# Performance work log

Measured on AMD Instinct MI355X. Metric: run time of the kernel, lower is better.

Reference implementation:

```python
import jax, jax.numpy as jnp
import numpy as np

B, S, H, E, V, OOV = 64, 400, 512, 256, 50000, 100

def setup_inputs() -> dict:
    key = jax.random.key(0)
    ks = jax.random.split(key, 32)
    p = lambda i, shape: jax.random.normal(ks[i], shape, jnp.float32) * 0.02
    emb = p(0, (V, E)).at[0].set(0.0)  # padding_idx=0
    return dict(
        summaries_in=jax.random.randint(ks[1], (B,), 1, V),
        h0=jax.random.normal(ks[2], (B, H), jnp.float32),
        c0=jax.random.normal(ks[3], (B, H), jnp.float32),
        encoder_out=jax.random.normal(ks[4], (B, S, 2 * H), jnp.float32),
        encoder_features=jax.random.normal(ks[5], (S * B, 2 * H), jnp.float32),
        encoder_mask=jnp.ones((S, B), jnp.float32),
        context=jax.random.normal(ks[6], (B, 2 * H), jnp.float32),
        coverage=jax.random.uniform(ks[7], (S, B), jnp.float32) * 0.01,
        texts_extended=jax.random.randint(ks[8], (S, B), 0, V + OOV),
        oov_size=OOV,
        emb=emb,
        W_feat=p(10, (2 * H, 2 * H)), b_feat=p(11, (2 * H,)),
        W_cov=p(12, (2 * H,)), b_cov=p(13, (2 * H,)),
        w_att=p(14, (2 * H,)), b_att=p(15, ()),
        W_ih=p(16, (4 * H, E)), W_hh=p(17, (4 * H, H)),
        b_ih=p(18, (4 * H,)), b_hh=p(19, (4 * H,)),
        W_ctx=p(20, (E, 2 * H + E)), b_ctx=p(21, (E,)),
        W_pg=p(22, (4 * H + E,)), b_pg=p(23, ()),
        W_o1=p(24, (H, 3 * H)), b_o1=p(25, (H,)),
        W_o2=p(26, (V, H)), b_o2=p(27, (V,)),
    )


def reference(summaries_in, h0, c0, encoder_out, encoder_features, encoder_mask,
              context, coverage, texts_extended, oov_size, emb,
              W_feat, b_feat, W_cov, b_cov, w_att, b_att,
              W_ih, W_hh, b_ih, b_hh, W_ctx, b_ctx, W_pg, b_pg,
              W_o1, b_o1, W_o2, b_o2):
    # embedding + context projection: [B, 2H+E] -> [B, E]
    x = emb[summaries_in]
    ctx_out = jnp.concatenate([context, x], axis=1) @ W_ctx.T + b_ctx
    # single LSTM step (torch gate order i, f, g, o)
    gates = ctx_out @ W_ih.T + b_ih + h0 @ W_hh.T + b_hh
    i, f, g, o = jnp.split(gates, 4, axis=1)
    c = jax.nn.sigmoid(f) * c0 + jax.nn.sigmoid(i) * jnp.tanh(g)
    h = jax.nn.sigmoid(o) * jnp.tanh(c)
    hidden_out = jnp.concatenate([h, c], axis=1)  # [B, 2H]
    # Bahdanau attention with coverage
    dec_feat = hidden_out @ W_feat.T + b_feat                 # [B, 2H]
    ef = encoder_features.reshape(S, B, 2 * H)                # [S, B, 2H]
    cov_feat = coverage[..., None] * W_cov + b_cov            # Linear(1, 2H)
    e = jnp.tanh(ef + dec_feat[None] + cov_feat) @ w_att + b_att  # [S, B]
    a = jax.nn.softmax(e, axis=0) * encoder_mask
    a = a / jnp.sum(a, axis=0, keepdims=True)                 # renormalize (Normalize(0))
    ctx_new = jnp.einsum('sb,bsd->bd', a, encoder_out)        # [B, 2H]
    coverage_next = coverage + a
    # pointer-generator mix
    gen_in = jnp.concatenate([ctx_new, hidden_out, ctx_out], axis=1)  # [B, 4H+E]
    p_gen = jax.nn.sigmoid(gen_in @ W_pg + b_pg)[:, None]             # [B, 1]
    logits = (jnp.concatenate([h, ctx_new], axis=1) @ W_o1.T + b_o1) @ W_o2.T + b_o2
    vocab_dist = p_gen * jax.nn.softmax(logits, axis=1)       # [B, V]
    attn_w = (1.0 - p_gen) * a.T                              # [B, S]
    vd = jnp.concatenate([vocab_dist, jnp.zeros((B, oov_size), vocab_dist.dtype)], axis=1)
    vd = vd.at[jnp.arange(B)[:, None], texts_extended.T].add(attn_w)  # scatter_add copy dist
    return vd, hidden_out, ctx_new, a, coverage_next
```

## Files before the change

### kernel.cpp

```cpp
#include <hip/hip_runtime.h>
#include <cmath>

#define B 64
#define S 400
#define H 512
#define E 256
#define V 50000
#define OOV 100
#define H2 1024
#define VDN (V + OOV)
#define NBLK_V 782

typedef __attribute__((ext_vector_type(8))) short short8;
typedef __attribute__((ext_vector_type(4))) float f32x4;

__device__ __forceinline__ float wred_sum(float v) {
#pragma unroll
  for (int o = 32; o > 0; o >>= 1) v += __shfl_down(v, o, 64);
  return v;
}
__device__ __forceinline__ float wred_max(float v) {
#pragma unroll
  for (int o = 32; o > 0; o >>= 1) v = fmaxf(v, __shfl_down(v, o, 64));
  return v;
}
__device__ __forceinline__ short f2bf(float f) {
  return __builtin_bit_cast(short, (__bf16)f);
}

__global__ __launch_bounds__(256) void k_init(const float* __restrict__ b_ctx,
                                              const float* __restrict__ b_ih,
                                              const float* __restrict__ b_hh,
                                              const float* __restrict__ b_feat,
                                              const float* __restrict__ b_o1,
                                              float* __restrict__ ctxoutT4,
                                              float* __restrict__ gates,
                                              float* __restrict__ dfeat,
                                              float* __restrict__ innerT4) {
  int idx = blockIdx.x * 256 + threadIdx.x;
  if (idx < 16384) {
    int j = ((idx >> 8) << 2) + (idx & 3);
    ctxoutT4[idx] = b_ctx[j];
  } else if (idx < 16384 + 131072) {
    int i = idx - 16384;
    int j = i & 2047;
    gates[i] = b_ih[j] + b_hh[j];
  } else if (idx < 16384 + 131072 + 65536) {
    int i = idx - 16384 - 131072;
    dfeat[i] = b_feat[i & 1023];
  } else {
    int i = idx - 16384 - 131072 - 65536;
    int j = ((i >> 8) << 2) + (i & 3);
    innerT4[i] = b_o1[j];
  }
}

__global__ __launch_bounds__(256) void k_pack(const float* __restrict__ context,
                                              const float* __restrict__ emb,
                                              const int* __restrict__ sumin,
                                              const float* __restrict__ h0,
                                              float* __restrict__ catT4,
                                              float* __restrict__ h0T4) {
  int idx = blockIdx.x * 256 + threadIdx.x;
  if (idx < 81920) {
    int e = idx & 3, b = (idx >> 2) & 63, q = idx >> 8;
    int k = q * 4 + e;
    catT4[idx] = (k < 1024) ? context[b * 1024 + k]
                            : emb[(size_t)sumin[b] * 256 + (k - 1024)];
  } else {
    int i = idx - 81920;
    int e = i & 3, b = (i >> 2) & 63, q = i >> 8;
    h0T4[i] = h0[b * 512 + q * 4 + e];
  }
}

template <int R, int KC, int OUTMODE>
__global__ __launch_bounds__(256) void k_gemmsk(
    const float* __restrict__ A1, const float* __restrict__ W1, int ldw1, int s1,
    const float* __restrict__ A2, const float* __restrict__ W2, int ldw2,
    float* __restrict__ out, int ldout) {
  const int lane = threadIdx.x;
  const int w = threadIdx.y;
  const int j0 = blockIdx.x * (4 * R) + w * R;
  const float* A;
  const float* W;
  int ldw, kc0;
  if ((int)blockIdx.y < s1) {
    A = A1; W = W1; ldw = ldw1; kc0 = blockIdx.y * KC;
  } else {
    A = A2; W = W2; ldw = ldw2; kc0 = (blockIdx.y - s1) * KC;
  }
  float acc[R];
#pragma unroll
  for (int r = 0; r < R; ++r) acc[r] = 0.f;
  const float* ap = A + (size_t)kc0 * 256 + lane * 4;
  const float* wr[R];
#pragma unroll
  for (int r = 0; r < R; ++r) wr[r] = W + (size_t)(j0 + r) * ldw + kc0 * 4;
#pragma unroll 8
  for (int k4 = 0; k4 < KC; ++k4) {
    float4 av = *(const float4*)(ap + (size_t)k4 * 256);
#pragma unroll
    for (int r = 0; r < R; ++r) {
      float4 wv = *(const float4*)(wr[r] + k4 * 4);
      acc[r] += av.x * wv.x + av.y * wv.y + av.z * wv.z + av.w * wv.w;
    }
  }
#pragma unroll
  for (int r = 0; r < R; ++r) {
    int j = j0 + r;
    if constexpr (OUTMODE == 0)
      atomicAdd(&out[((size_t)(j >> 2) * 64 + lane) * 4 + (j & 3)], acc[r]);
    else
      atomicAdd(&out[(size_t)lane * ldout + j], acc[r]);
  }
}

__global__ __launch_bounds__(256) void k_lstm(const float* __restrict__ gates,
                                              const float* __restrict__ c0,
                                              float* __restrict__ hidden,
                                              float* __restrict__ hcT4) {
  int idx = blockIdx.x * 256 + threadIdx.x;
  int b = idx >> 9, u = idx & 511;
  float gi = gates[(size_t)b * 2048 + u];
  float gf = gates[(size_t)b * 2048 + 512 + u];
  float gg = gates[(size_t)b * 2048 + 1024 + u];
  float go = gates[(size_t)b * 2048 + 1536 + u];
  float si = 1.f / (1.f + expf(-gi));
  float sf = 1.f / (1.f + expf(-gf));
  float so = 1.f / (1.f + expf(-go));
  float c = sf * c0[(size_t)b * 512 + u] + si * tanhf(gg);
  float h = so * tanhf(c);
  hidden[(size_t)b * H2 + u] = h;
  hidden[(size_t)b * H2 + 512 + u] = c;
  hcT4[((u >> 2) * 64 + b) * 4 + (u & 3)] = h;
  int k = 512 + u;
  hcT4[((k >> 2) * 64 + b) * 4 + (k & 3)] = c;
}

__global__ __launch_bounds__(128) void k_e(
    const float* __restrict__ ef, const float* __restrict__ dfeat,
    const float* __restrict__ cov, const float* __restrict__ Wcov,
    const float* __restrict__ bcov, const float* __restrict__ watt,
    const float* __restrict__ batt, float* __restrict__ e_out) {
  const int sb = blockIdx.x;
  const int b = sb & 63;
  const float cval = cov[sb];
  const float4* efr = (const float4*)(ef + (size_t)sb * H2);
  const float4* dfr = (const float4*)(dfeat + (size_t)b * H2);
  const float4* wcr = (const float4*)Wcov;
  const float4* bcr = (const float4*)bcov;
  const float4* war = (const float4*)watt;
  float sum = 0.f;
#pragma unroll
  for (int i = 0; i < 2; ++i) {
    int d4 = threadIdx.x + i * 128;
    float4 ev = efr[d4], dv = dfr[d4], wc = wcr[d4], bc = bcr[d4], wa = war[d4];
    sum += tanhf(ev.x + dv.x + cval * wc.x + bc.x) * wa.x;
    sum += tanhf(ev.y + dv.y + cval * wc.y + bc.y) * wa.y;
    sum += tanhf(ev.z + dv.z + cval * wc.z + bc.z) * wa.z;
    sum += tanhf(ev.w + dv.w + cval * wc.w + bc.w) * wa.w;
  }
  sum = wred_sum(sum);
  __shared__ float ls[2];
  if ((threadIdx.x & 63) == 0) ls[threadIdx.x >> 6] = sum;
  __syncthreads();
  if (threadIdx.x == 0) e_out[sb] = ls[0] + ls[1] + batt[0];
}

__global__ __launch_bounds__(512) void k_soft(const float* __restrict__ e,
                                              const float* __restrict__ mask,
                                              const float* __restrict__ cov_in,
                                              float* __restrict__ a_out,
                                              float* __restrict__ cov_out) {
  const int b = blockIdx.x;
  const int s = threadIdx.x;
  __shared__ float red[8];
  float ev = (s < S) ? e[s * B + b] : -INFINITY;
  float m = wred_max(ev);
  if ((s & 63) == 0) red[s >> 6] = m;
  __syncthreads();
  if (s == 0) {
    float mm = red[0];
#pragma unroll
    for (int i = 1; i < 8; ++i) mm = fmaxf(mm, red[i]);
    red[0] = mm;
  }
  __syncthreads();
  m = red[0];
  float ex = (s < S) ? mask[s * B + b] * expf(ev - m) : 0.f;
  float ws = wred_sum(ex);
  __syncthreads();
  if ((s & 63) == 0) red[s >> 6] = ws;
  __syncthreads();
  if (s == 0) {
    float z = 0.f;
#pragma unroll
    for (int i = 0; i < 8; ++i) z += red[i];
    red[0] = z;
  }
  __syncthreads();
  float Z = red[0];
  if (s < S) {
    float av = ex / Z;
    a_out[s * B + b] = av;
    cov_out[s * B + b] = cov_in[s * B + b] + av;
  }
}

__global__ __launch_bounds__(256) void k_ctxp(const float* __restrict__ a,
                                              const float* __restrict__ enc,
                                              float* __restrict__ part) {
  const int b = blockIdx.x & 63;
  const int sc = blockIdx.x >> 6;
  const int d = threadIdx.x * 4;
  float4 acc = make_float4(0.f, 0.f, 0.f, 0.f);
  for (int s = sc * 25; s < sc * 25 + 25; ++s) {
    float av = a[s * B + b];
    float4 ev = *(const float4*)(enc + ((size_t)b * S + s) * H2 + d);
    acc.x += av * ev.x;
    acc.y += av * ev.y;
    acc.z += av * ev.z;
    acc.w += av * ev.w;
  }
  *(float4*)(part + (size_t)blockIdx.x * H2 + d) = acc;
}

__global__ __launch_bounds__(256) void k_ctxred(const float* __restrict__ part,
                                                float* __restrict__ ctx_new,
                                                float* __restrict__ ctxT4) {
  int idx = blockIdx.x * 256 + threadIdx.x;
  float s = 0.f;
#pragma unroll
  for (int sc = 0; sc < 16; ++sc) s += part[(size_t)sc * 65536 + idx];
  int b = idx >> 10, d = idx & 1023;
  ctx_new[idx] = s;
  ctxT4[((d >> 2) * 64 + b) * 4 + (d & 3)] = s;
}

__global__ __launch_bounds__(256) void k_pgen(
    const float* __restrict__ ctx_new, const float* __restrict__ hidden,
    const float* __restrict__ ctxoutT4, const float* __restrict__ Wpg,
    const float* __restrict__ bpg, float* __restrict__ pgen) {
  const int b = blockIdx.x;
  float p = 0.f;
  for (int k = threadIdx.x; k < 2304; k += 256) {
    float v;
    if (k < 1024) v = ctx_new[(size_t)b * H2 + k];
    else if (k < 2048) v = hidden[(size_t)b * H2 + k - 1024];
    else {
      int ko = k - 2048;
      v = ctxoutT4[((ko >> 2) * 64 + b) * 4 + (ko & 3)];
    }
    p += v * Wpg[k];
  }
  p = wred_sum(p);
  __shared__ float red[4];
  if ((threadIdx.x & 63) == 0) red[threadIdx.x >> 6] = p;
  __syncthreads();
  if (threadIdx.x == 0) {
    float d = red[0] + red[1] + red[2] + red[3] + bpg[0];
    pgen[b] = 1.f / (1.f + expf(-d));
  }
}

__global__ __launch_bounds__(256) void k_packinner(const float* __restrict__ innerT4,
                                                   short8* __restrict__ packB) {
  int f = blockIdx.x * 256 + threadIdx.x;
  int l = f & 63, bt = (f >> 6) & 3, ks = f >> 8;
  int b = bt * 16 + (l & 15);
  int kbase = ks * 32 + (l >> 4) * 8;
  float4 q0 = *(const float4*)&innerT4[(size_t)(kbase / 4) * 256 + b * 4];
  float4 q1 = *(const float4*)&innerT4[(size_t)(kbase / 4 + 1) * 256 + b * 4];
  short8 frag;
  frag[0] = f2bf(q0.x); frag[1] = f2bf(q0.y);
  frag[2] = f2bf(q0.z); frag[3] = f2bf(q0.w);
  frag[4] = f2bf(q1.x); frag[5] = f2bf(q1.y);
  frag[6] = f2bf(q1.z); frag[7] = f2bf(q1.w);
  packB[f] = frag;
}

__global__ __launch_bounds__(256) void k_mfma_logits(
    const float* __restrict__ W2, const short8* __restrict__ packB,
    const float* __restrict__ bias, float* __restrict__ logits,
    float* __restrict__ mp, float* __restrict__ zp) {
  const int l = threadIdx.x;
  const int w = threadIdx.y;
  const int jblk = blockIdx.x * 64;
  const int jw = jblk + w * 16;
  const int jv = min(jw + (l & 15), V - 1);
  const float* wp = W2 + (size_t)jv * 512 + (l >> 4) * 8;

  f32x4 acc0 = {0.f, 0.f, 0.f, 0.f}, acc1 = acc0, acc2 = acc0, acc3 = acc0;
#pragma unroll 2
  for (int ks = 0; ks < 16; ++ks) {
    float4 w0 = *(const float4*)&wp[ks * 32];
    float4 w1 = *(const float4*)&wp[ks * 32 + 4];
    short8 af;
    af[0] = f2bf(w0.x); af[1] = f2bf(w0.y); af[2] = f2bf(w0.z); af[3] = f2bf(w0.w);
    af[4] = f2bf(w1.x); af[5] = f2bf(w1.y); af[6] = f2bf(w1.z); af[7] = f2bf(w1.w);
    short8 b0 = packB[(ks * 4 + 0) * 64 + l];
    short8 b1 = packB[(ks * 4 + 1) * 64 + l];
    short8 b2 = packB[(ks * 4 + 2) * 64 + l];
    short8 b3 = packB[(ks * 4 + 3) * 64 + l];
    acc0 = __builtin_amdgcn_mfma_f32_16x16x32_bf16(af, b0, acc0, 0, 0, 0);
    acc1 = __builtin_amdgcn_mfma_f32_16x16x32_bf16(af, b1, acc1, 0, 0, 0);
    acc2 = __builtin_amdgcn_mfma_f32_16x16x32_bf16(af, b2, acc2, 0, 0, 0);
    acc3 = __builtin_amdgcn_mfma_f32_16x16x32_bf16(af, b3, acc3, 0, 0, 0);
  }

  __shared__ float tile[64][65];
  const int rbase = w * 16 + (l >> 4) * 4;
#pragma unroll
  for (int v = 0; v < 4; ++v) {
    int jl = rbase + v;
    int j = jblk + jl;
    float bv = bias[min(j, V - 1)];
    bool valid = (j < V);
    tile[jl][0 * 16 + (l & 15)] = valid ? acc0[v] + bv : -INFINITY;
    tile[jl][1 * 16 + (l & 15)] = valid ? acc1[v] + bv : -INFINITY;
    tile[jl][2 * 16 + (l & 15)] = valid ? acc2[v] + bv : -INFINITY;
    tile[jl][3 * 16 + (l & 15)] = valid ? acc3[v] + bv : -INFINITY;
  }
  __syncthreads();
  const int t = w * 64 + l;
#pragma unroll
  for (int i = 0; i < 16; ++i) {
    int idx = i * 256 + t;
    int jl = idx & 63;
    int b = idx >> 6;
    int j = jblk + jl;
    if (j < V) logits[(size_t)b * V + j] = tile[jl][b];
  }
  if (t < 64) {
    float m = -INFINITY;
#pragma unroll
    for (int jl = 0; jl < 64; ++jl) m = fmaxf(m, tile[jl][t]);
    float z = 0.f;
#pragma unroll
    for (int jl = 0; jl < 64; ++jl) z += expf(tile[jl][t] - m);
    mp[(size_t)blockIdx.x * 64 + t] = m;
    zp[(size_t)blockIdx.x * 64 + t] = z;
  }
}

__global__ __launch_bounds__(256) void k_vdm(const float* __restrict__ logits,
                                             const float* __restrict__ mp,
                                             const float* __restrict__ zp,
                                             const float* __restrict__ pgen,
                                             float* __restrict__ out) {
  const int b = blockIdx.x >> 3;
  const int c = blockIdx.x & 7;
  const int t = threadIdx.x;
  __shared__ float red[4];
  float m = -INFINITY;
  for (int i = t; i < NBLK_V; i += 256) m = fmaxf(m, mp[i * 64 + b]);
  m = wred_max(m);
  if ((t & 63) == 0) red[t >> 6] = m;
  __syncthreads();
  const float M = fmaxf(fmaxf(red[0], red[1]), fmaxf(red[2], red[3]));
  float z = 0.f;
  for (int i = t; i < NBLK_V; i += 256) z += zp[i * 64 + b] * expf(mp[i * 64 + b] - M);
  z = wred_sum(z);
  __syncthreads();
  if ((t & 63) == 0) red[t >> 6] = z;
  __syncthreads();
  const float Z = red[0] + red[1] + red[2] + red[3];
  const float scale = pgen[b] / Z;
  const int v0 = c * 6272;
  const int v1 = min(v0 + 6272, VDN);
  for (int v = v0 + t; v < v1; v += 256) {
    float val = (v < V) ? scale * expf(logits[(size_t)b * V + v] - M) : 0.f;
    out[(size_t)b * VDN + v] = val;
  }
}

__global__ __launch_bounds__(256) void k_scatter(const float* __restrict__ a,
                                                 const int* __restrict__ tex,
                                                 const float* __restrict__ pgen,
                                                 float* __restrict__ vd) {
  int g = blockIdx.x * 256 + threadIdx.x;
  if (g >= S * B) return;
  int b = g & 63;
  float w = (1.f - pgen[b]) * a[g];
  atomicAdd(&vd[(size_t)b * VDN + tex[g]], w);
}

extern "C" void kernel_launch(void* const* d_in, const int* in_sizes, int n_in,
                              void* d_out, int out_size, void* d_ws, size_t ws_size,
                              hipStream_t stream) {
  const int* sumin = (const int*)d_in[0];
  const float* h0 = (const float*)d_in[1];
  const float* c0 = (const float*)d_in[2];
  const float* enc_out = (const float*)d_in[3];
  const float* ef = (const float*)d_in[4];
  const float* mask = (const float*)d_in[5];
  const float* context = (const float*)d_in[6];
  const float* coverage = (const float*)d_in[7];
  const int* tex = (const int*)d_in[8];
  const float* emb = (const float*)d_in[10];
  const float* W_feat = (const float*)d_in[11];
  const float* b_feat = (const float*)d_in[12];
  const float* W_cov = (const float*)d_in[13];
  const float* b_cov = (const float*)d_in[14];
  const float* w_att = (const float*)d_in[15];
  const float* b_att = (const float*)d_in[16];
  const float* W_ih = (const float*)d_in[17];
  const float* W_hh = (const float*)d_in[18];
  const float* b_ih = (const float*)d_in[19];
  const float* b_hh = (const float*)d_in[20];
  const float* W_ctx = (const float*)d_in[21];
  const float* b_ctx = (const float*)d_in[22];
  const float* W_pg = (const float*)d_in[23];
  const float* b_pg = (const float*)d_in[24];
  const float* W_o1 = (const float*)d_in[25];
  const float* b_o1 = (const float*)d_in[26];
  const float* W_o2 = (const float*)d_in[27];
  const float* b_o2 = (const float*)d_in[28];

  float* out = (float*)d_out;
  float* vd = out;
  float* hidden = vd + (size_t)B * VDN;
  float* ctx_new = hidden + (size_t)B * H2;
  float* a_out = ctx_new + (size_t)B * H2;
  float* cov_out = a_out + (size_t)S * B;

  float* ws = (float*)d_ws;
  float* catT4 = ws;
  float* h0T4 = catT4 + 81920;
  float* ctxoutT4 = h0T4 + 32768;
  float* gates = ctxoutT4 + 16384;
  float* hidcatT4 = gates + 131072;
  float* dfeat = hidcatT4 + 65536;
  float* e_ws = dfeat + 65536;
  float* ctxnewT4 = e_ws + 25600;
  float* innerT4 = ctxnewT4 + 65536;
  float* pgen = innerT4 + 32768;
  float* mp = pgen + 64;
  float* zp = mp + 50048;
  float* packBf = zp + 50048;
  float* logits = packBf + 16384;
  float* part = logits;
  short8* packB = (short8*)packBf;

  dim3 gblk(64, 4);

  k_init<<<960, 256, 0, stream>>>(b_ctx, b_ih, b_hh, b_feat, b_o1, ctxoutT4,
                                  gates, dfeat, innerT4);
  k_pack<<<448, 256, 0, stream>>>(context, emb, sumin, h0, catT4, h0T4);
  k_gemmsk<2, 64, 0><<<dim3(32, 5), gblk, 0, stream>>>(
      catT4, W_ctx, 1280, 5, nullptr, nullptr, 0, ctxoutT4, 0);
  k_gemmsk<2, 64, 1><<<dim3(256, 3), gblk, 0, stream>>>(
      ctxoutT4, W_ih, 256, 1, h0T4, W_hh, 512, gates, 2048);
  k_lstm<<<128, 256, 0, stream>>>(gates, c0, hidden, hidcatT4);
  k_gemmsk<2, 64, 1><<<dim3(128, 4), gblk, 0, stream>>>(
      hidcatT4, W_feat, 1024, 4, nullptr, nullptr, 0, dfeat, 1024);
  k_e<<<S * B, 128, 0, stream>>>(ef, dfeat, coverage, W_cov, b_cov, w_att, b_att, e_ws);
  k_soft<<<B, 512, 0, stream>>>(e_ws, mask, coverage, a_out, cov_out);
  k_ctxp<<<16 * B, 256, 0, stream>>>(a_out, enc_out, part);
  k_ctxred<<<256, 256, 0, stream>>>(part, ctx_new, ctxnewT4);
  k_pgen<<<B, 256, 0, stream>>>(ctx_new, hidden, ctxoutT4, W_pg, b_pg, pgen);
  k_gemmsk<2, 64, 0><<<dim3(64, 6), gblk, 0, stream>>>(
      hidcatT4, W_o1, 1536, 2, ctxnewT4, W_o1 + 512, 1536, innerT4, 0);
  k_packinner<<<16, 256, 0, stream>>>(innerT4, packB);
  k_mfma_logits<<<NBLK_V, gblk, 0, stream>>>(W_o2, packB, b_o2, logits, mp, zp);
  k_vdm<<<B * 8, 256, 0, stream>>>(logits, mp, zp, pgen, vd);
  k_scatter<<<100, 256, 0, stream>>>(a_out, tex, pgen, vd);
}
```

Baseline: 223.4 us.

## Prefetch encoder features and W_o2 into cache via extra blocks in earlier kernels

Extra blocks are appended to each small, latency-bound kernel. These blocks stream later-needed tensors (encoder_features, encoder_out, W_o2) through the cache so subsequent kernels find them resident in L2 or MALL. k_init and k_pack are merged into a single k_pre launch. k_e now processes two (s,b) rows per 256-thread block. The gemm kernels switch to a flattened 1D grid so prefetch blocks can be appended. The risk is that prefetch traffic competes with the real work for bandwidth, and that data gets evicted before use if caches are too small.

```diff
diff --git a/kernel.cpp b/kernel.cpp
--- a/kernel.cpp
+++ b/kernel.cpp
@@ -27,16 +27,28 @@
 __device__ __forceinline__ short f2bf(float f) {
   return __builtin_bit_cast(short, (__bf16)f);
 }
-
-__global__ __launch_bounds__(256) void k_init(const float* __restrict__ b_ctx,
-                                              const float* __restrict__ b_ih,
-                                              const float* __restrict__ b_hh,
-                                              const float* __restrict__ b_feat,
-                                              const float* __restrict__ b_o1,
-                                              float* __restrict__ ctxoutT4,
-                                              float* __restrict__ gates,
-                                              float* __restrict__ dfeat,
-                                              float* __restrict__ innerT4) {
+__device__ __forceinline__ void pf_run(const float4* __restrict__ pf, int pf_n4,
+                                       int pb, int npb, int t, int T) {
+  for (int i = pb * T + t; i < pf_n4; i += npb * T) {
+    float4 v = pf[i];
+    asm volatile("" ::"v"(v.x), "v"(v.y), "v"(v.z), "v"(v.w));
+  }
+}
+
+__global__ __launch_bounds__(256) void k_pre(
+    const float* __restrict__ b_ctx, const float* __restrict__ b_ih,
+    const float* __restrict__ b_hh, const float* __restrict__ b_feat,
+    const float* __restrict__ b_o1, const float* __restrict__ context,
+    const float* __restrict__ emb, const int* __restrict__ sumin,
+    const float* __restrict__ h0, float* __restrict__ ctxoutT4,
+    float* __restrict__ gates, float* __restrict__ dfeat,
+    float* __restrict__ innerT4, float* __restrict__ catT4,
+    float* __restrict__ h0T4, const float4* __restrict__ pf, int pf_n4) {
+  const int NW = 1408;
+  if ((int)blockIdx.x >= NW) {
+    pf_run(pf, pf_n4, blockIdx.x - NW, gridDim.x - NW, threadIdx.x, 256);
+    return;
+  }
   int idx = blockIdx.x * 256 + threadIdx.x;
   if (idx < 16384) {
     int j = ((idx >> 8) << 2) + (idx & 3);
@@ -48,27 +60,18 @@
   } else if (idx < 16384 + 131072 + 65536) {
     int i = idx - 16384 - 131072;
     dfeat[i] = b_feat[i & 1023];
-  } else {
+  } else if (idx < 245760) {
     int i = idx - 16384 - 131072 - 65536;
     int j = ((i >> 8) << 2) + (i & 3);
     innerT4[i] = b_o1[j];
-  }
-}
-
-__global__ __launch_bounds__(256) void k_pack(const float* __restrict__ context,
-                                              const float* __restrict__ emb,
-                                              const int* __restrict__ sumin,
-                                              const float* __restrict__ h0,
-                                              float* __restrict__ catT4,
-                                              float* __restrict__ h0T4) {
-  int idx = blockIdx.x * 256 + threadIdx.x;
-  if (idx < 81920) {
-    int e = idx & 3, b = (idx >> 2) & 63, q = idx >> 8;
+  } else if (idx < 245760 + 81920) {
+    int i = idx - 245760;
+    int e = i & 3, b = (i >> 2) & 63, q = i >> 8;
     int k = q * 4 + e;
-    catT4[idx] = (k < 1024) ? context[b * 1024 + k]
-                            : emb[(size_t)sumin[b] * 256 + (k - 1024)];
+    catT4[i] = (k < 1024) ? context[b * 1024 + k]
+                          : emb[(size_t)sumin[b] * 256 + (k - 1024)];
   } else {
-    int i = idx - 81920;
+    int i = idx - 245760 - 81920;
     int e = i & 3, b = (i >> 2) & 63, q = i >> 8;
     h0T4[i] = h0[b * 512 + q * 4 + e];
   }
@@ -78,17 +81,26 @@
 __global__ __launch_bounds__(256) void k_gemmsk(
     const float* __restrict__ A1, const float* __restrict__ W1, int ldw1, int s1,
     const float* __restrict__ A2, const float* __restrict__ W2, int ldw2,
-    float* __restrict__ out, int ldout) {
+    float* __restrict__ out, int ldout, int jblks, int stot,
+    const float4* __restrict__ pf, int pf_n4) {
   const int lane = threadIdx.x;
   const int w = threadIdx.y;
-  const int j0 = blockIdx.x * (4 * R) + w * R;
+  const int t = w * 64 + lane;
+  const int nwork = jblks * stot;
+  if ((int)blockIdx.x >= nwork) {
+    pf_run(pf, pf_n4, blockIdx.x - nwork, gridDim.x - nwork, t, 256);
+    return;
+  }
+  const int jb = blockIdx.x % jblks;
+  const int y = blockIdx.x / jblks;
+  const int j0 = jb * (4 * R) + w * R;
   const float* A;
   const float* W;
   int ldw, kc0;
-  if ((int)blockIdx.y < s1) {
-    A = A1; W = W1; ldw = ldw1; kc0 = blockIdx.y * KC;
+  if (y < s1) {
+    A = A1; W = W1; ldw = ldw1; kc0 = y * KC;
   } else {
-    A = A2; W = W2; ldw = ldw2; kc0 = (blockIdx.y - s1) * KC;
+    A = A2; W = W2; ldw = ldw2; kc0 = (y - s1) * KC;
   }
   float acc[R];
 #pragma unroll
@@ -119,7 +131,13 @@
 __global__ __launch_bounds__(256) void k_lstm(const float* __restrict__ gates,
                                               const float* __restrict__ c0,
                                               float* __restrict__ hidden,
-                                              float* __restrict__ hcT4) {
+                                              float* __restrict__ hcT4,
+                                              const float4* __restrict__ pf,
+                                              int pf_n4) {
+  if ((int)blockIdx.x >= 128) {
+    pf_run(pf, pf_n4, blockIdx.x - 128, gridDim.x - 128, threadIdx.x, 256);
+    return;
+  }
   int idx = blockIdx.x * 256 + threadIdx.x;
   int b = idx >> 9, u = idx & 511;
   float gi = gates[(size_t)b * 2048 + u];
@@ -138,12 +156,19 @@
   hcT4[((k >> 2) * 64 + b) * 4 + (k & 3)] = c;
 }
 
-__global__ __launch_bounds__(128) void k_e(
+__global__ __launch_bounds__(256) void k_e(
     const float* __restrict__ ef, const float* __restrict__ dfeat,
     const float* __restrict__ cov, const float* __restrict__ Wcov,
     const float* __restrict__ bcov, const float* __restrict__ watt,
-    const float* __restrict__ batt, float* __restrict__ e_out) {
-  const int sb = blockIdx.x;
+    const float* __restrict__ batt, float* __restrict__ e_out,
+    const float4* __restrict__ pf, int pf_n4) {
+  const int t = threadIdx.x;
+  if ((int)blockIdx.x >= 12800) {
+    pf_run(pf, pf_n4, blockIdx.x - 12800, gridDim.x - 12800, t, 256);
+    return;
+  }
+  const int half = t >> 7, tid = t & 127;
+  const int sb = blockIdx.x * 2 + half;
   const int b = sb & 63;
   const float cval = cov[sb];
   const float4* efr = (const float4*)(ef + (size_t)sb * H2);
@@ -154,7 +179,7 @@
   float sum = 0.f;
 #pragma unroll
   for (int i = 0; i < 2; ++i) {
-    int d4 = threadIdx.x + i * 128;
+    int d4 = tid + i * 128;
     float4 ev = efr[d4], dv = dfr[d4], wc = wcr[d4], bc = bcr[d4], wa = war[d4];
     sum += tanhf(ev.x + dv.x + cval * wc.x + bc.x) * wa.x;
     sum += tanhf(ev.y + dv.y + cval * wc.y + bc.y) * wa.y;
@@ -162,17 +187,23 @@
     sum += tanhf(ev.w + dv.w + cval * wc.w + bc.w) * wa.w;
   }
   sum = wred_sum(sum);
-  __shared__ float ls[2];
-  if ((threadIdx.x & 63) == 0) ls[threadIdx.x >> 6] = sum;
-  __syncthreads();
-  if (threadIdx.x == 0) e_out[sb] = ls[0] + ls[1] + batt[0];
+  __shared__ float ls[4];
+  if ((t & 63) == 0) ls[t >> 6] = sum;
+  __syncthreads();
+  if (tid == 0) e_out[sb] = ls[2 * half] + ls[2 * half + 1] + batt[0];
 }
 
 __global__ __launch_bounds__(512) void k_soft(const float* __restrict__ e,
                                               const float* __restrict__ mask,
                                               const float* __restrict__ cov_in,
                                               float* __restrict__ a_out,
-                                              float* __restrict__ cov_out) {
+                                              float* __restrict__ cov_out,
+                                              const float4* __restrict__ pf,
+                                              int pf_n4) {
+  if ((int)blockIdx.x >= B) {
+    pf_run(pf, pf_n4, blockIdx.x - B, gridDim.x - B, threadIdx.x, 512);
+    return;
+  }
   const int b = blockIdx.x;
   const int s = threadIdx.x;
   __shared__ float red[8];
@@ -210,7 +241,13 @@
 
 __global__ __launch_bounds__(256) void k_ctxp(const float* __restrict__ a,
                                               const float* __restrict__ enc,
-                                              float* __restrict__ part) {
+                                              float* __restrict__ part,
+                                              const float4* __restrict__ pf,
+                                              int pf_n4) {
+  if ((int)blockIdx.x >= 1024) {
+    pf_run(pf, pf_n4, blockIdx.x - 1024, gridDim.x - 1024, threadIdx.x, 256);
+    return;
+  }
   const int b = blockIdx.x & 63;
   const int sc = blockIdx.x >> 6;
   const int d = threadIdx.x * 4;
@@ -228,7 +265,13 @@
 
 __global__ __launch_bounds__(256) void k_ctxred(const float* __restrict__ part,
                                                 float* __restrict__ ctx_new,
-                                                float* __restrict__ ctxT4) {
+                                                float* __restrict__ ctxT4,
+                                                const float4* __restrict__ pf,
+                                                int pf_n4) {
+  if ((int)blockIdx.x >= 256) {
+    pf_run(pf, pf_n4, blockIdx.x - 256, gridDim.x - 256, threadIdx.x, 256);
+    return;
+  }
   int idx = blockIdx.x * 256 + threadIdx.x;
   float s = 0.f;
 #pragma unroll
@@ -241,7 +284,12 @@
 __global__ __launch_bounds__(256) void k_pgen(
     const float* __restrict__ ctx_new, const float* __restrict__ hidden,
     const float* __restrict__ ctxoutT4, const float* __restrict__ Wpg,
-    const float* __restrict__ bpg, float* __restrict__ pgen) {
+    const float* __restrict__ bpg, float* __restrict__ pgen,
+    const float4* __restrict__ pf, int pf_n4) {
+  if ((int)blockIdx.x >= B) {
+    pf_run(pf, pf_n4, blockIdx.x - B, gridDim.x - B, threadIdx.x, 256);
+    return;
+  }
   const int b = blockIdx.x;
   float p = 0.f;
   for (int k = threadIdx.x; k < 2304; k += 256) {
@@ -265,7 +313,13 @@
 }
 
 __global__ __launch_bounds__(256) void k_packinner(const float* __restrict__ innerT4,
-                                                   short8* __restrict__ packB) {
+                                                   short8* __restrict__ packB,
+                                                   const float4* __restrict__ pf,
+                                                   int pf_n4) {
+  if ((int)blockIdx.x >= 16) {
+    pf_run(pf, pf_n4, blockIdx.x - 16, gridDim.x - 16, threadIdx.x, 256);
+    return;
+  }
   int f = blockIdx.x * 256 + threadIdx.x;
   int l = f & 63, bt = (f >> 6) & 3, ks = f >> 8;
   int b = bt * 16 + (l & 15);
@@ -443,26 +497,45 @@
   float* part = logits;
   short8* packB = (short8*)packBf;
 
+  const float4* ef4 = (const float4*)ef;
+  const float4* enc4 = (const float4*)enc_out;
+  const float4* wo24 = (const float4*)W_o2;
+  const int EFS = 1310720;
+  const int WOS = 1066672;
+  const int WOL = 6400000 - 5 * WOS;
+
   dim3 gblk(64, 4);
 
-  k_init<<<960, 256, 0, stream>>>(b_ctx, b_ih, b_hh, b_feat, b_o1, ctxoutT4,
-                                  gates, dfeat, innerT4);
-  k_pack<<<448, 256, 0, stream>>>(context, emb, sumin, h0, catT4, h0T4);
-  k_gemmsk<2, 64, 0><<<dim3(32, 5), gblk, 0, stream>>>(
-      catT4, W_ctx, 1280, 5, nullptr, nullptr, 0, ctxoutT4, 0);
-  k_gemmsk<2, 64, 1><<<dim3(256, 3), gblk, 0, stream>>>(
-      ctxoutT4, W_ih, 256, 1, h0T4, W_hh, 512, gates, 2048);
-  k_lstm<<<128, 256, 0, stream>>>(gates, c0, hidden, hidcatT4);
-  k_gemmsk<2, 64, 1><<<dim3(128, 4), gblk, 0, stream>>>(
-      hidcatT4, W_feat, 1024, 4, nullptr, nullptr, 0, dfeat, 1024);
-  k_e<<<S * B, 128, 0, stream>>>(ef, dfeat, coverage, W_cov, b_cov, w_att, b_att, e_ws);
-  k_soft<<<B, 512, 0, stream>>>(e_ws, mask, coverage, a_out, cov_out);
-  k_ctxp<<<16 * B, 256, 0, stream>>>(a_out, enc_out, part);
-  k_ctxred<<<256, 256, 0, stream>>>(part, ctx_new, ctxnewT4);
-  k_pgen<<<B, 256, 0, stream>>>(ctx_new, hidden, ctxoutT4, W_pg, b_pg, pgen);
-  k_gemmsk<2, 64, 0><<<dim3(64, 6), gblk, 0, stream>>>(
-      hidcatT4, W_o1, 1536, 2, ctxnewT4, W_o1 + 512, 1536, innerT4, 0);
-  k_packinner<<<16, 256, 0, stream>>>(innerT4, packB);
+  k_pre<<<1408 + 256, 256, 0, stream>>>(b_ctx, b_ih, b_hh, b_feat, b_o1,
+                                        context, emb, sumin, h0, ctxoutT4, gates,
+                                        dfeat, innerT4, catT4, h0T4,
+                                        ef4 + 0 * EFS, EFS);
+  k_gemmsk<2, 64, 0><<<160 + 256, gblk, 0, stream>>>(
+      catT4, W_ctx, 1280, 5, nullptr, nullptr, 0, ctxoutT4, 0, 32, 5,
+      ef4 + 1 * EFS, EFS);
+  k_gemmsk<2, 64, 1><<<768 + 256, gblk, 0, stream>>>(
+      ctxoutT4, W_ih, 256, 1, h0T4, W_hh, 512, gates, 2048, 256, 3,
+      ef4 + 2 * EFS, EFS);
+  k_lstm<<<128 + 256, 256, 0, stream>>>(gates, c0, hidden, hidcatT4,
+                                        ef4 + 3 * EFS, EFS);
+  k_gemmsk<2, 64, 1><<<512 + 256, gblk, 0, stream>>>(
+      hidcatT4, W_feat, 1024, 4, nullptr, nullptr, 0, dfeat, 1024, 128, 4,
+      ef4 + 4 * EFS, EFS);
+  k_e<<<12800 + 256, 256, 0, stream>>>(ef, dfeat, coverage, W_cov, b_cov, w_att,
+                                       b_att, e_ws, enc4, 6553600);
+  k_soft<<<B + 256, 512, 0, stream>>>(e_ws, mask, coverage, a_out, cov_out,
+                                      wo24 + 0 * WOS, WOS);
+  k_ctxp<<<1024 + 256, 256, 0, stream>>>(a_out, enc_out, part,
+                                         wo24 + 1 * WOS, WOS);
+  k_ctxred<<<256 + 256, 256, 0, stream>>>(part, ctx_new, ctxnewT4,
+                                          wo24 + 2 * WOS, WOS);
+  k_pgen<<<B + 256, 256, 0, stream>>>(ctx_new, hidden, ctxoutT4, W_pg, b_pg,
+                                      pgen, wo24 + 3 * WOS, WOS);
+  k_gemmsk<2, 64, 0><<<384 + 256, gblk, 0, stream>>>(
+      hidcatT4, W_o1, 1536, 2, ctxnewT4, W_o1 + 512, 1536, innerT4, 0, 64, 6,
+      wo24 + 4 * WOS, WOS);
+  k_packinner<<<16 + 128, 256, 0, stream>>>(innerT4, packB,
+                                            wo24 + 5 * WOS, WOL);
   k_mfma_logits<<<NBLK_V, gblk, 0, stream>>>(W_o2, packB, b_o2, logits, mp, zp);
   k_vdm<<<B * 8, 256, 0, stream>>>(logits, mp, zp, pgen, vd);
   k_scatter<<<100, 256, 0, stream>>>(a_out, tex, pgen, vd);
```

After: 300.3 us. 1.34x slower.
